# Kernel tuning notes

Hardware: AMD Instinct MI355X
Metric: run time of the kernel (lower is better)

Reference implementation:

```python
import jax, jax.numpy as jnp
import numpy as np

B_GR = 128    # graphs per batch
N0 = 512      # nodes per graph before pooling
E_PER = 4096  # edges per graph (kept static; pooled-away edges get weight 0)
H = 128       # hidden
F = 128       # num_features (== hidden)
C = 10        # num_classes
K_HOP = 3     # Jacobi polynomial order (hop_num)
A_J, B_J = 1.0, 1.0
EPS = 1e-5


def _bn(h, g, b):
    # training-mode BatchNorm1d: batch stats, biased variance
    m = jnp.mean(h, 0)
    v = jnp.mean((h - m) ** 2, 0)
    return (h - m) * jax.lax.rsqrt(v + EPS) * g + b


def _forward(x, convW, convb, bnW, bnB, bn7W, bn7B, attW, theta,
             lin1W, lin1b, lin2W, lin2b, lin3W, lin3b, src, dst):
    w = jnp.ones((src.shape[0],), x.dtype)  # edge weights; 0 => filtered edge
    n = N0
    h = x
    reads = []
    for i in range(5):
        N = B_GR * n
        # symmetric GCN normalization with self loops on the weighted graph
        deg = jax.ops.segment_sum(w, dst, num_segments=N) + 1.0
        dinv = jax.lax.rsqrt(deg)
        enorm = dinv[src] * dinv[dst] * w   # per-edge norm [E]
        snorm = dinv * dinv                 # self-loop norm [N]
        prop = lambda m_: jax.ops.segment_sum(enorm[:, None] * m_[src], dst, num_segments=N) + m_ * snorm[:, None]
        pvec = lambda v_: jax.ops.segment_sum(enorm * v_[src], dst, num_segments=N) + v_ * snorm
        # GCNConv -> BN -> ReLU
        h = prop(h @ convW[i]) + convb[i]
        h = jax.nn.relu(_bn(h, bnW[i], bnB[i]))
        # JacobiPool: Jacobi-polynomial diffusion of attention scores
        s0 = h @ attW[i]                    # [N]
        polys = [s0, 0.5 * ((A_J - B_J) * s0 + (A_J + B_J + 2.0) * pvec(s0))]
        for kk in range(2, K_HOP + 1):
            c0 = 2 * kk * (kk + A_J + B_J) * (2 * kk + A_J + B_J - 2)
            c1 = (2 * kk + A_J + B_J - 1) * (2 * kk + A_J + B_J) * (2 * kk + A_J + B_J - 2)
            c2 = (2 * kk + A_J + B_J - 1) * (A_J * A_J - B_J * B_J)
            c3 = 2 * (kk + A_J - 1) * (kk + B_J - 1) * (2 * kk + A_J + B_J)
            polys.append((c1 * pvec(polys[-1]) + c2 * polys[-1] - c3 * polys[-2]) / c0)
        score = sum(theta[i, j] * polys[j] for j in range(K_HOP + 1))
        # top-k node selection per graph (ratio 0.5 -> static k)
        k = n // 2
        _, idx = jax.lax.top_k(score.reshape(B_GR, n), k)
        sel = (idx + (jnp.arange(B_GR) * n)[:, None]).reshape(-1)  # global node ids [B*k]
        h = h[sel] * jnp.tanh(score[sel])[:, None]
        # remap/filter edges to surviving nodes (masked, static edge count)
        new_id = jnp.full((N,), -1, jnp.int32).at[sel].set(jnp.arange(B_GR * k, dtype=jnp.int32))
        ns, nd = new_id[src], new_id[dst]
        valid = (ns >= 0) & (nd >= 0) & (w > 0)
        w = valid.astype(x.dtype)
        src = jnp.where(valid, ns, 0)
        dst = jnp.where(valid, nd, 0)
        # readout: global max pool || global mean pool per graph
        xg = h.reshape(B_GR, k, H)
        reads.append(jnp.concatenate([xg.max(1), xg.mean(1)], -1))
        n = k
    g = sum(reads) / 5.0                    # [B, 2H]
    g = jax.nn.relu(_bn(g @ lin1W + lin1b, bnW[5], bnB[5]))
    g = jax.nn.relu(_bn(g @ lin2W + lin2b, bn7W, bn7B))
    return jax.nn.log_softmax(g @ lin3W + lin3b, -1)


def setup_inputs() -> dict:
    key = jax.random.key(0)
    ks = jax.random.split(key, 8)
    N = B_GR * N0
    E = B_GR * E_PER
    rng = np.random.default_rng(0)
    off = np.repeat(np.arange(B_GR, dtype=np.int32) * N0, E_PER)
    src = jnp.asarray(off + rng.integers(0, N0, E).astype(np.int32))
    dst = jnp.asarray(off + rng.integers(0, N0, E).astype(np.int32))
    s = 1.0 / np.sqrt(H)
    return {
        "x": jax.random.normal(ks[0], (N, F), jnp.float32),
        "convW": jax.random.normal(ks[1], (5, H, H), jnp.float32) * s,
        "convb": jnp.zeros((5, H), jnp.float32),
        "bnW": jnp.ones((6, H), jnp.float32),
        "bnB": jnp.zeros((6, H), jnp.float32),
        "bn7W": jnp.ones((H // 2,), jnp.float32),
        "bn7B": jnp.zeros((H // 2,), jnp.float32),
        "attW": jax.random.normal(ks[2], (5, H), jnp.float32) * s,
        "theta": jax.random.normal(ks[3], (5, K_HOP + 1), jnp.float32) * 0.5,
        "lin1W": jax.random.normal(ks[4], (2 * H, H), jnp.float32) * (1.0 / np.sqrt(2 * H)),
        "lin1b": jnp.zeros((H,), jnp.float32),
        "lin2W": jax.random.normal(ks[5], (H, H // 2), jnp.float32) * s,
        "lin2b": jnp.zeros((H // 2,), jnp.float32),
        "lin3W": jax.random.normal(ks[6], (H // 2, C), jnp.float32) * (1.0 / np.sqrt(H // 2)),
        "lin3b": jnp.zeros((C,), jnp.float32),
        "src": src,
        "dst": dst,
    }


def reference(x, convW, convb, bnW, bnB, bn7W, bn7B, attW, theta,
              lin1W, lin1b, lin2W, lin2b, lin3W, lin3b, src, dst):
    return _forward(x, convW, convb, bnW, bnB, bn7W, bn7B, attW, theta,
                    lin1W, lin1b, lin2W, lin2b, lin3W, lin3b, src, dst)
```

## Files before the change

kernel.cpp:

```cpp
#include <hip/hip_runtime.h>
#include <hip/hip_bf16.h>

#define B_GRAPH 128
#define ETOT    (128*4096)
#define N0G     (128*512)
#define HF      128
#define STSZ    2048

union IGSmem {
    float Ws[64*HF];
    struct { int cnt8[8][512]; int cur[512]; float dvl[512]; int wsum[4]; } ini;
};

__global__ __launch_bounds__(256) void k_init_gemm(
    const float* __restrict__ A, const float* __restrict__ Wg, float* __restrict__ C,
    const int* __restrict__ s_in, const int* __restrict__ d_in_,
    int2* __restrict__ csr, int2* __restrict__ rb2, float* __restrict__ dinvv,
    float* __restrict__ gacc, float* __restrict__ statsH,
    float* __restrict__ st0, float* __restrict__ st1, float* __restrict__ st2)
{
    __shared__ IGSmem sm;
    int t = threadIdx.x;
    if (blockIdx.x >= 128){
        int tx = t & 15, ty = t >> 4;
        int r0 = (blockIdx.x - 128)*128 + ty*8, c0 = tx*4;
        float acc[8][8];
        #pragma unroll
        for (int j=0;j<8;++j)
            #pragma unroll
            for (int l=0;l<8;++l) acc[j][l] = 0.f;
        for (int kh = 0; kh < 2; ++kh){
            __syncthreads();
            {
                float4* d4 = (float4*)sm.Ws;
                const float4* s4 = (const float4*)(Wg + kh*64*HF);
                #pragma unroll
                for (int i2 = 0; i2 < 8; ++i2) d4[t + i2*256] = s4[t + i2*256];
            }
            __syncthreads();
            float4 avc[8];
            #pragma unroll
            for (int j=0;j<8;++j)
                avc[j] = *(const float4*)(A + (size_t)(r0+j)*HF + kh*64);
            for (int k4 = 0; k4 < 16; ++k4){
                int k4n = (k4+1 < 16) ? (k4+1) : 15;
                float4 avn[8];
                #pragma unroll
                for (int j=0;j<8;++j)
                    avn[j] = *(const float4*)(A + (size_t)(r0+j)*HF + kh*64 + k4n*4);
                #pragma unroll
                for (int kk=0; kk<4; ++kk){
                    int kl = k4*4 + kk;
                    float4 w0 = *(const float4*)(sm.Ws + kl*HF + c0);
                    float4 w1 = *(const float4*)(sm.Ws + kl*HF + c0 + 64);
                    #pragma unroll
                    for (int j=0;j<8;++j){
                        float a = reinterpret_cast<const float*>(&avc[j])[kk];
                        acc[j][0] += a*w0.x; acc[j][1] += a*w0.y; acc[j][2] += a*w0.z; acc[j][3] += a*w0.w;
                        acc[j][4] += a*w1.x; acc[j][5] += a*w1.y; acc[j][6] += a*w1.z; acc[j][7] += a*w1.w;
                    }
                }
                #pragma unroll
                for (int j=0;j<8;++j) avc[j] = avn[j];
            }
        }
        #pragma unroll
        for (int j=0;j<8;++j){
            *(float4*)(C + (size_t)(r0+j)*HF + c0)      = make_float4(acc[j][0],acc[j][1],acc[j][2],acc[j][3]);
            *(float4*)(C + (size_t)(r0+j)*HF + c0 + 64) = make_float4(acc[j][4],acc[j][5],acc[j][6],acc[j][7]);
        }
    } else {
        int g = blockIdx.x;
        int wid = t >> 5;
        for (int l = t; l < 4096; l += 256) ((int*)sm.ini.cnt8)[l] = 0;
        gacc[g*256 + t] = 0.f;
        if (g == 0){
            if (t < 256){ statsH[t] = 0.f; if (t < 128) statsH[256+t] = 0.f; }
            for (int i = t; i < STSZ; i += 256){ st0[i] = 0.f; st1[i] = 0.f; st2[i] = 0.f; }
        }
        __syncthreads();
        for (int j = t; j < 4096; j += 256){
            int e = g*4096 + j;
            atomicAdd(&sm.ini.cnt8[wid][d_in_[e] & 511], 1);
        }
        __syncthreads();
        int c0 = 0, c1 = 0;
        #pragma unroll
        for (int w = 0; w < 8; ++w){ c0 += sm.ini.cnt8[w][2*t]; c1 += sm.ini.cnt8[w][2*t+1]; }
        int pairsum = c0 + c1;
        int lane = t & 63, wv = t >> 6;
        int v = pairsum;
        #pragma unroll
        for (int off = 1; off < 64; off <<= 1){
            int nv = __shfl_up(v, off);
            if (lane >= off) v += nv;
        }
        if (lane == 63) sm.ini.wsum[wv] = v;
        __syncthreads();
        for (int ww = 0; ww < wv; ++ww) v += sm.ini.wsum[ww];
        int begpair = v - pairsum;
        sm.ini.cur[2*t]   = begpair;
        sm.ini.cur[2*t+1] = begpair + c0;
        sm.ini.cnt8[0][2*t]   = c0;
        sm.ini.cnt8[0][2*t+1] = c1;
        __syncthreads();
        for (int l = t; l < 512; l += 256){
            int cl = sm.ini.cnt8[0][l];
            rb2[g*512 + l] = make_int2(g*4096 + sm.ini.cur[l], cl);
            float dv = rsqrtf((float)cl + 1.f);
            sm.ini.dvl[l] = dv;
            dinvv[g*512 + l] = dv;
        }
        __syncthreads();
        for (int j = t; j < 4096; j += 256){
            int e = g*4096 + j;
            int sg = s_in[e], dl = d_in_[e] & 511;
            int p = atomicAdd(&sm.ini.cur[dl], 1);
            csr[g*4096 + (p & 4095)] = make_int2(sg, __float_as_int(sm.ini.dvl[sg & 511]));
        }
    }
}

template<int NN>
__global__ __launch_bounds__(512) void k_prop_lds(
    const float* __restrict__ Y, const float* __restrict__ cb,
    const int2* __restrict__ rb2, const int2* __restrict__ cp,
    const float* __restrict__ dinv, float* __restrict__ X, float* __restrict__ st)
{
    constexpr int TP = 512 / NN;
    constexpr int FQ = 8 / TP;
    __shared__ float4 ly[NN * 8];
    int b = blockIdx.x;
    int g = b >> 2, q = b & 3;
    int t = threadIdx.x;
    const float4* Y4 = (const float4*)Y + (size_t)g*NN*32 + q*8;
    for (int i = t; i < NN*8; i += 512){
        int row = i >> 3, slot = i & 7;
        ly[row*8 + ((slot + row) & 7)] = Y4[(size_t)row*32 + slot];
    }
    __syncthreads();
    int r   = t & (NN - 1);
    int sub = t / NN;
    int S0  = sub * FQ;
    int vg  = g*NN + r;
    float dv = dinv[vg];
    int2 rb = rb2[vg];
    int e0  = (rb.x - g*4096) & 4095;
    int len = min(max(rb.y, 0), 4096 - e0);
    const int2* cpg = cp + g*4096 + e0;
    float4 acc[FQ];
    #pragma unroll
    for (int s = 0; s < FQ; ++s) acc[s] = make_float4(0.f,0.f,0.f,0.f);
    for (int j = 0; j < len; ++j){
        int2 e = cpg[j];
        int c = e.x & (NN - 1);
        float en = __int_as_float(e.y);
        #pragma unroll
        for (int s = 0; s < FQ; ++s){
            float4 h = ly[c*8 + ((S0 + s + c) & 7)];
            acc[s].x += en*h.x; acc[s].y += en*h.y; acc[s].z += en*h.z; acc[s].w += en*h.w;
        }
    }
    const float4* cb4 = (const float4*)cb + q*8;
    float4* X4 = (float4*)X + q*8;
    #pragma unroll
    for (int s = 0; s < FQ; ++s){
        float4 y = ly[r*8 + ((S0 + s + r) & 7)];
        float4 cbv = cb4[S0 + s];
        acc[s].x = y.x*dv*dv + dv*acc[s].x + cbv.x;
        acc[s].y = y.y*dv*dv + dv*acc[s].y + cbv.y;
        acc[s].z = y.z*dv*dv + dv*acc[s].z + cbv.z;
        acc[s].w = y.w*dv*dv + dv*acc[s].w + cbv.w;
        X4[(size_t)vg*32 + S0 + s] = acc[s];
    }
    __syncthreads();
    float* lf = (float*)ly;
    #pragma unroll
    for (int s = 0; s < FQ; ++s) *(float4*)&lf[r*32 + (S0 + s)*4] = acc[s];
    __syncthreads();
    float ssum = 0.f, qsum = 0.f;
    {
        int col = t & 31, grp = t >> 5;
        for (int rr = grp; rr < NN; rr += 16){
            float v = lf[rr*32 + col];
            ssum += v; qsum += v*v;
        }
    }
    __syncthreads();
    lf[t] = ssum; lf[512 + t] = qsum;
    __syncthreads();
    if (t < 64){
        int col = t & 31, half = t >> 5;
        float a = 0.f;
        #pragma unroll
        for (int i = 0; i < 16; ++i) a += lf[half*512 + i*32 + col];
        atomicAdd(&st[(b & 7)*256 + half*128 + q*32 + col], a);
    }
}

__global__ __launch_bounds__(256) void k_prop_stats(const float* __restrict__ Y, const float* __restrict__ cb,
                                                    const int2* __restrict__ rb2, const int2* __restrict__ cp,
                                                    const float* __restrict__ dinv,
                                                    float* __restrict__ X, float* __restrict__ st,
                                                    int n, int lb, int Nn){
    __shared__ float rs[1024], rq[1024];
    int xcd = blockIdx.x & 7, c = blockIdx.x >> 3;
    int g = xcd*16 + (c >> lb);
    int m = c & ((1 << lb) - 1);
    int nd = threadIdx.x >> 5;
    int v = g*n + m*8 + nd;
    int f4 = threadIdx.x & 31;
    float dv = dinv[v];
    float4 y = *(const float4*)(Y + (size_t)v*HF + f4*4);
    float4 acc = make_float4(0.f, 0.f, 0.f, 0.f);
    int2 rb = rb2[v];
    int len = min(max(rb.y, 0), 4096);
    int e0 = rb.x, e1 = rb.x + len;
    for (int j = e0; j < e1; ++j){
        int2 e = cp[j];
        int s = e.x & (Nn - 1);
        float en = __int_as_float(e.y);
        float4 h = *(const float4*)(Y + (size_t)s*HF + f4*4);
        acc.x += en*h.x; acc.y += en*h.y; acc.z += en*h.z; acc.w += en*h.w;
    }
    int f = f4*4;
    acc.x = y.x*dv*dv + dv*acc.x + cb[f];
    acc.y = y.y*dv*dv + dv*acc.y + cb[f+1];
    acc.z = y.z*dv*dv + dv*acc.z + cb[f+2];
    acc.w = y.w*dv*dv + dv*acc.w + cb[f+3];
    *(float4*)(X + (size_t)v*HF + f) = acc;
    *(float4*)&rs[nd*HF + f] = acc;
    *(float4*)&rq[nd*HF + f] = make_float4(acc.x*acc.x, acc.y*acc.y, acc.z*acc.z, acc.w*acc.w);
    __syncthreads();
    if (threadIdx.x < 128){
        int tt = threadIdx.x;
        float s = 0.f, q = 0.f;
        #pragma unroll
        for (int j = 0; j < 8; ++j){ s += rs[j*HF + tt]; q += rq[j*HF + tt]; }
        atomicAdd(&st[xcd*256 + tt], s);
        atomicAdd(&st[xcd*256 + 128 + tt], q);
    }
}

__global__ __launch_bounds__(256) void k_score(
    const float* __restrict__ H, const float* __restrict__ stats,
    const float* __restrict__ gw, const float* __restrict__ gb,
    const float* __restrict__ aw, float* __restrict__ s0G, float invN)
{
    __shared__ float bna[128], bnb[128], awl[128];
    int t = threadIdx.x;
    if (t < 128){
        float s = 0.f, q = 0.f;
        #pragma unroll
        for (int b2 = 0; b2 < 8; ++b2){ s += stats[b2*256 + t]; q += stats[b2*256 + 128 + t]; }
        float mean = s*invN;
        float var  = q*invN - mean*mean;
        float iv   = rsqrtf(var + 1e-5f);
        bna[t] = iv*gw[t];
        bnb[t] = gb[t] - mean*iv*gw[t];
        awl[t] = aw[t];
    }
    __syncthreads();
    int v = blockIdx.x*128 + (t >> 1);
    int h = t & 1;
    const float* hp = H + (size_t)v*HF + h*64;
    float part = 0.f;
    #pragma unroll
    for (int j = 0; j < 16; ++j){
        float4 x = *(const float4*)(hp + j*4);
        int f = h*64 + j*4;
        float4 a4 = *(const float4*)&bna[f];
        float4 b4 = *(const float4*)&bnb[f];
        float4 w4 = *(const float4*)&awl[f];
        part += fmaxf(x.x*a4.x + b4.x, 0.f)*w4.x
              + fmaxf(x.y*a4.y + b4.y, 0.f)*w4.y
              + fmaxf(x.z*a4.z + b4.z, 0.f)*w4.z
              + fmaxf(x.w*a4.w + b4.w, 0.f)*w4.w;
    }
    float oth = __shfl_xor(part, 1);
    if (h == 0) s0G[v] = part + oth;
}

__global__ __launch_bounds__(256) void k_gemm_g(
    const float* __restrict__ Hsrc, const float* __restrict__ stats,
    const float* __restrict__ gw, const float* __restrict__ gb,
    const int* __restrict__ siG, const float* __restrict__ tssG,
    const float* __restrict__ Wg, float* __restrict__ C,
    float invN, int lk, int ln)
{
    __shared__ float Ws[64*HF];
    __shared__ float bna[128], bnb[128];
    int t = threadIdx.x;
    if (t < 128){
        float s = 0.f, q = 0.f;
        #pragma unroll
        for (int b2 = 0; b2 < 8; ++b2){ s += stats[b2*256 + t]; q += stats[b2*256 + 128 + t]; }
        float mean = s*invN;
        float var  = q*invN - mean*mean;
        float iv   = rsqrtf(var + 1e-5f);
        bna[t] = iv*gw[t];
        bnb[t] = gb[t] - mean*iv*gw[t];
    }
    int tx = t & 15, ty = t >> 4;
    int r0 = blockIdx.x*128 + ty*8, c0 = tx*4;
    int rbase[8]; float ts_[8];
    int nmask = (1 << ln) - 1;
    #pragma unroll
    for (int j = 0; j < 8; ++j){
        int rg = r0 + j;
        int g = rg >> lk;
        int old = siG[rg] & nmask;
        rbase[j] = ((g << ln) + old) * HF;
        ts_[j] = tssG[rg];
    }
    float acc[8][8];
    #pragma unroll
    for (int j=0;j<8;++j)
        #pragma unroll
        for (int l=0;l<8;++l) acc[j][l] = 0.f;
    for (int kh = 0; kh < 2; ++kh){
        __syncthreads();
        {
            float4* d4 = (float4*)Ws;
            const float4* s4 = (const float4*)(Wg + kh*64*HF);
            #pragma unroll
            for (int i2 = 0; i2 < 8; ++i2) d4[t + i2*256] = s4[t + i2*256];
        }
        __syncthreads();
        float4 avc[8];
        #pragma unroll
        for (int j=0;j<8;++j) avc[j] = *(const float4*)(Hsrc + (size_t)rbase[j] + kh*64);
        for (int k4 = 0; k4 < 16; ++k4){
            int fb  = kh*64 + k4*4;
            int fbn = kh*64 + (((k4+1 < 16) ? (k4+1) : 15) * 4);
            float4 avn[8];
            #pragma unroll
            for (int j=0;j<8;++j) avn[j] = *(const float4*)(Hsrc + (size_t)rbase[j] + fbn);
            float4 ba = *(const float4*)&bna[fb];
            float4 bb = *(const float4*)&bnb[fb];
            #pragma unroll
            for (int j=0;j<8;++j){
                avc[j].x = fmaxf(avc[j].x*ba.x + bb.x, 0.f)*ts_[j];
                avc[j].y = fmaxf(avc[j].y*ba.y + bb.y, 0.f)*ts_[j];
                avc[j].z = fmaxf(avc[j].z*ba.z + bb.z, 0.f)*ts_[j];
                avc[j].w = fmaxf(avc[j].w*ba.w + bb.w, 0.f)*ts_[j];
            }
            #pragma unroll
            for (int kk=0; kk<4; ++kk){
                int kl = k4*4 + kk;
                float4 w0 = *(const float4*)(Ws + kl*HF + c0);
                float4 w1 = *(const float4*)(Ws + kl*HF + c0 + 64);
                #pragma unroll
                for (int j=0;j<8;++j){
                    float a = reinterpret_cast<const float*>(&avc[j])[kk];
                    acc[j][0] += a*w0.x; acc[j][1] += a*w0.y; acc[j][2] += a*w0.z; acc[j][3] += a*w0.w;
                    acc[j][4] += a*w1.x; acc[j][5] += a*w1.y; acc[j][6] += a*w1.z; acc[j][7] += a*w1.w;
                }
            }
            #pragma unroll
            for (int j=0;j<8;++j) avc[j] = avn[j];
        }
    }
    #pragma unroll
    for (int j=0;j<8;++j){
        *(float4*)(C + (size_t)(r0+j)*HF + c0)      = make_float4(acc[j][0],acc[j][1],acc[j][2],acc[j][3]);
        *(float4*)(C + (size_t)(r0+j)*HF + c0 + 64) = make_float4(acc[j][4],acc[j][5],acc[j][6],acc[j][7]);
    }
}

struct __align__(16) PSmem {
    int2  eds[4096];
    int2  rbl[512];
    float dvv[512], p0[512], p1[512], p2[512];
    float ss[512]; int si[512]; float tss[256]; int nid[512];
    int   cnt_[256]; int wsum[4]; float dvn[256];
    float bna[128], bnb[128]; float red[1024];
};

__global__ __launch_bounds__(1024) void k_pool(
    const float* __restrict__ H, const float* __restrict__ stats,
    const float* __restrict__ gw, const float* __restrict__ gb,
    const float* __restrict__ th,
    const int2* __restrict__ rb2, int2* __restrict__ csr, const float* __restrict__ dinv,
    const float* __restrict__ s0G,
    float* __restrict__ gacc, int2* __restrict__ rb2n, float* __restrict__ dinvn,
    float* __restrict__ stZero, int* __restrict__ siG, float* __restrict__ tssG,
    const float* __restrict__ lin1W, const float* __restrict__ lin1b,
    float* __restrict__ t1g, float* __restrict__ statsH,
    float invN, float ca2, float cc2, float ca3, float cc3,
    int n, int last)
{
    int g = blockIdx.x, t = threadIdx.x;
    int k = n >> 1;
    __shared__ PSmem sm;

    if (t < 256) stZero[(g & 7)*256 + t] = 0.f;
    if (t < 128){
        float s = 0.f, q = 0.f;
        #pragma unroll
        for (int b2 = 0; b2 < 8; ++b2){ s += stats[b2*256 + t]; q += stats[b2*256 + 128 + t]; }
        float mean = s*invN;
        float var  = q*invN - mean*mean;
        float iv   = rsqrtf(var + 1e-5f);
        sm.bna[t] = iv*gw[t];
        sm.bnb[t] = gb[t] - mean*iv*gw[t];
    }
    for (int l = t; l < n; l += 1024){
        int2 rb = rb2[g*n + l];
        int bx = (rb.x - g*4096) & 4095;
        int by = min(max(rb.y, 0), 4096 - bx);
        sm.rbl[l] = make_int2(bx, by);
        sm.dvv[l] = dinv[g*n + l];
        sm.p0[l]  = s0G[g*n + l];
    }
    __syncthreads();
    int medg = sm.rbl[n-1].x + sm.rbl[n-1].y;
    for (int j = t; j < medg; j += 1024){
        int2 e = csr[g*4096 + j];
        sm.eds[j] = make_int2(e.x & (n-1), e.y);
    }
    __syncthreads();
    for (int l = t; l < n; l += 1024){
        int2 rc = sm.rbl[l];
        float acc = 0.f;
        for (int j = 0; j < rc.y; ++j){
            int2 e = sm.eds[rc.x + j];
            acc += __int_as_float(e.y) * sm.p0[e.x];
        }
        float dv = sm.dvv[l];
        sm.p1[l] = 2.f*(sm.p0[l]*dv*dv + dv*acc);
    }
    __syncthreads();
    for (int l = t; l < n; l += 1024){
        int2 rc = sm.rbl[l];
        float acc = 0.f;
        for (int j = 0; j < rc.y; ++j){
            int2 e = sm.eds[rc.x + j];
            acc += __int_as_float(e.y) * sm.p1[e.x];
        }
        float dv = sm.dvv[l];
        sm.p2[l] = ca2*(sm.p1[l]*dv*dv + dv*acc) + cc2*sm.p0[l];
    }
    __syncthreads();
    float t0v = th[0], t1v = th[1], t2c = th[2], t3v = th[3];
    for (int l = t; l < n; l += 1024){
        int2 rc = sm.rbl[l];
        float acc = 0.f;
        for (int j = 0; j < rc.y; ++j){
            int2 e = sm.eds[rc.x + j];
            acc += __int_as_float(e.y) * sm.p2[e.x];
        }
        float dv = sm.dvv[l];
        float tv = sm.p2[l]*dv*dv + dv*acc;
        float p3 = ca3*tv + cc3*sm.p1[l];
        sm.ss[l] = t0v*sm.p0[l] + t1v*sm.p1[l] + t2c*sm.p2[l] + t3v*p3;
    }
    __syncthreads();
    for (int l = t; l < n; l += 1024){
        float sl = sm.ss[l];
        int r = 0;
        for (int j = 0; j < n; j += 4){
            float4 s4 = *(const float4*)&sm.ss[j];
            r += (s4.x > sl) || (s4.x == sl && (j    ) < l);
            r += (s4.y > sl) || (s4.y == sl && (j + 1) < l);
            r += (s4.z > sl) || (s4.z == sl && (j + 2) < l);
            r += (s4.w > sl) || (s4.w == sl && (j + 3) < l);
        }
        if (r < k){
            sm.nid[l] = r;
            sm.si[r]  = l;
            float tv = tanhf(sl);
            sm.tss[r] = tv;
            siG[g*k + r]  = l;
            tssG[g*k + r] = tv;
        } else {
            sm.nid[l] = -1;
        }
    }
    __syncthreads();
    if (!last){
        if (t < k){
            int l = sm.si[t] & (n-1);
            int2 rc = sm.rbl[l];
            int c2 = 0;
            for (int j = 0; j < rc.y; ++j) c2 += (sm.nid[sm.eds[rc.x + j].x] >= 0);
            sm.cnt_[t] = c2;
        }
        __syncthreads();
        int c = (t < 256) ? ((t < k) ? sm.cnt_[t] : 0) : 0;
        int vscan = c;
        if (t < 256){
            int lane = t & 63;
            #pragma unroll
            for (int off = 1; off < 64; off <<= 1){
                int nv = __shfl_up(vscan, off);
                if (lane >= off) vscan += nv;
            }
            if (lane == 63) sm.wsum[t >> 6] = vscan;
        }
        __syncthreads();
        int beg = 0;
        if (t < k){
            int wv = t >> 6;
            int add = 0;
            for (int ww = 0; ww < wv; ++ww) add += sm.wsum[ww];
            vscan += add;
            beg = vscan - c;
            rb2n[g*k + t] = make_int2(g*4096 + beg, c);
            float dv = rsqrtf((float)c + 1.f);
            dinvn[g*k + t] = dv;
            sm.dvn[t] = dv;
        }
        __syncthreads();
        if (t < k){
            int l = sm.si[t] & (n-1);
            int2 rc = sm.rbl[l];
            int p = beg;
            for (int j = 0; j < rc.y; ++j){
                int ns = sm.nid[sm.eds[rc.x + j].x];
                if (ns >= 0){ csr[g*4096 + (p & 4095)] = make_int2(g*k + ns, __float_as_int(sm.dvn[ns])); ++p; }
            }
        }
        __syncthreads();
    }
    {
        int f4 = t & 31, rl = t >> 5;
        int f = f4*4;
        float4 a4 = *(const float4*)&sm.bna[f];
        float4 b4 = *(const float4*)&sm.bnb[f];
        float4 mx = make_float4(-3.4e38f,-3.4e38f,-3.4e38f,-3.4e38f);
        float4 smv = make_float4(0.f,0.f,0.f,0.f);
        for (int r = rl; r < k; r += 32){
            int old = sm.si[r] & (n-1);
            float4 hv = *(const float4*)(H + ((size_t)g*n + old)*HF + f);
            float ts = sm.tss[r];
            float4 v;
            v.x = fmaxf(hv.x*a4.x + b4.x, 0.f)*ts;
            v.y = fmaxf(hv.y*a4.y + b4.y, 0.f)*ts;
            v.z = fmaxf(hv.z*a4.z + b4.z, 0.f)*ts;
            v.w = fmaxf(hv.w*a4.w + b4.w, 0.f)*ts;
            mx.x = fmaxf(mx.x, v.x); mx.y = fmaxf(mx.y, v.y);
            mx.z = fmaxf(mx.z, v.z); mx.w = fmaxf(mx.w, v.w);
            smv.x += v.x; smv.y += v.y; smv.z += v.z; smv.w += v.w;
        }
        float* scr = (float*)sm.eds;
        *(float4*)&scr[rl*128 + f]        = mx;
        *(float4*)&scr[4096 + rl*128 + f] = smv;
        __syncthreads();
        if (t < 128){
            float m = -3.4e38f, s = 0.f;
            #pragma unroll
            for (int j = 0; j < 32; ++j){
                m = fmaxf(m, scr[j*128 + t]);
                s += scr[4096 + j*128 + t];
            }
            gacc[g*256 + t] += m;
            gacc[g*256 + 128 + t] += s / (float)k;
        }
    }
    if (last){
        __syncthreads();
        int c = t & 127, h = t >> 7;
        float s = 0.f;
        int k0 = h*32;
        #pragma unroll
        for (int kk = 0; kk < 32; ++kk)
            s += gacc[g*256 + k0 + kk] * lin1W[(k0 + kk)*128 + c];
        sm.red[t] = s;
        __syncthreads();
        if (t < 512) sm.red[t] += sm.red[t+512];
        __syncthreads();
        if (t < 256) sm.red[t] += sm.red[t+256];
        __syncthreads();
        if (t < 128){
            float v = (sm.red[t] + sm.red[t+128]) * 0.2f + lin1b[t];
            t1g[g*128 + t] = v;
            atomicAdd(&statsH[t], v);
            atomicAdd(&statsH[128+t], v*v);
        }
    }
}

__global__ __launch_bounds__(128) void k_head2(const float* __restrict__ t1, const float* __restrict__ gw,
                                               const float* __restrict__ gb, const float* __restrict__ W2,
                                               const float* __restrict__ b2, float* __restrict__ sh,
                                               float* __restrict__ t2){
    int r = blockIdx.x, t = threadIdx.x;
    int cc = t & 63, h = t >> 6;
    __shared__ float row[128];
    __shared__ float red[128];
    {
        float mean = sh[t] * (1.f/128.f);
        float var  = sh[128+t]*(1.f/128.f) - mean*mean;
        float iv   = rsqrtf(var + 1e-5f);
        float v = (t1[r*128+t] - mean)*iv*gw[t] + gb[t];
        row[t] = fmaxf(v, 0.f);
    }
    __syncthreads();
    float s = 0.f;
    #pragma unroll
    for (int kk = 0; kk < 64; ++kk)
        s += row[h*64+kk] * W2[(h*64+kk)*64 + cc];
    red[t] = s;
    __syncthreads();
    if (h == 0){
        float v = red[cc] + red[cc+64] + b2[cc];
        t2[r*64+cc] = v;
        atomicAdd(&sh[256+cc], v);
        atomicAdd(&sh[320+cc], v*v);
    }
}
__global__ __launch_bounds__(64) void k_head3(const float* __restrict__ t2, const float* __restrict__ gw,
                                              const float* __restrict__ gb, const float* __restrict__ W3,
                                              const float* __restrict__ b3, const float* __restrict__ sh,
                                              float* __restrict__ out){
    int r = blockIdx.x, t = threadIdx.x;
    float mean = sh[256+t]*(1.f/128.f);
    float var  = sh[320+t]*(1.f/128.f) - mean*mean;
    float iv   = rsqrtf(var + 1e-5f);
    float v = fmaxf((t2[r*64+t]-mean)*iv*gw[t] + gb[t], 0.f);
    float lg[10];
    #pragma unroll
    for (int j = 0; j < 10; ++j){
        float p = v * W3[t*10 + j];
        for (int off = 32; off; off >>= 1) p += __shfl_down(p, off);
        lg[j] = p;
    }
    if (t == 0){
        float m = -3.4e38f;
        #pragma unroll
        for (int j = 0; j < 10; ++j){ lg[j] += b3[j]; m = fmaxf(m, lg[j]); }
        float se = 0.f;
        #pragma unroll
        for (int j = 0; j < 10; ++j) se += expf(lg[j] - m);
        float l = logf(se) + m;
        #pragma unroll
        for (int j = 0; j < 10; ++j) out[r*10 + j] = lg[j] - l;
    }
}

extern "C" void kernel_launch(void* const* d_in, const int* in_sizes, int n_in,
                              void* d_out, int out_size, void* d_ws, size_t ws_size,
                              hipStream_t stream){
    const float* x     = (const float*)d_in[0];
    const float* convW = (const float*)d_in[1];
    const float* convb = (const float*)d_in[2];
    const float* bnW   = (const float*)d_in[3];
    const float* bnB   = (const float*)d_in[4];
    const float* bn7W  = (const float*)d_in[5];
    const float* bn7B  = (const float*)d_in[6];
    const float* attW  = (const float*)d_in[7];
    const float* theta = (const float*)d_in[8];
    const float* lin1W = (const float*)d_in[9];
    const float* lin1b = (const float*)d_in[10];
    const float* lin2W = (const float*)d_in[11];
    const float* lin2b = (const float*)d_in[12];
    const float* lin3W = (const float*)d_in[13];
    const float* lin3b = (const float*)d_in[14];
    const int*   src0  = (const int*)d_in[15];
    const int*   dst0  = (const int*)d_in[16];

    char* base = (char*)d_ws;
    size_t off = 0;
    auto take = [&](size_t bytes) -> void* {
        void* p = base + off;
        off = (off + bytes + 255) & ~(size_t)255;
        return p;
    };
    float* bufGP = (float*)take((size_t)N0G*HF*4);
    float* bufHA = (float*)take((size_t)N0G*HF*4);
    float* bufHB = (float*)take((size_t)(N0G/2)*HF*4);
    int2*  csr_p = (int2*) take((size_t)ETOT*8);
    int2*  rb2A  = (int2*) take((size_t)N0G*8);
    int2*  rb2B  = (int2*) take((size_t)N0G*8);
    float* dinvA = (float*)take((size_t)N0G*4);
    float* dinvB = (float*)take((size_t)N0G*4);
    float* s0G   = (float*)take((size_t)N0G*4);
    int*   siG   = (int*)  take((size_t)(N0G/2)*4);
    float* tssG  = (float*)take((size_t)(N0G/2)*4);
    float* st[3];
    st[0] = (float*)take(STSZ*4);
    st[1] = (float*)take(STSZ*4);
    st[2] = (float*)take(STSZ*4);
    float* gacc  = (float*)take((size_t)B_GRAPH*256*4);
    float* t1    = (float*)take((size_t)B_GRAPH*128*4);
    float* t2    = (float*)take((size_t)B_GRAPH*64*4);
    float* statsH= (float*)take(384*4);

    auto coef = [](int kk, float& ca, float& cc){
        double a = 1.0, b = 1.0;
        double c0 = 2.0*kk*(kk+a+b)*(2.0*kk+a+b-2.0);
        double c1 = (2.0*kk+a+b-1.0)*(2.0*kk+a+b)*(2.0*kk+a+b-2.0);
        double c3 = 2.0*(kk+a-1.0)*(kk+b-1.0)*(2.0*kk+a+b);
        ca = (float)(c1/c0); cc = (float)(-c3/c0);
    };
    float ca2, cc2, ca3, cc3;
    coef(2, ca2, cc2);
    coef(3, ca3, cc3);

    k_init_gemm<<<128 + 512, 256, 0, stream>>>(x, convW, bufGP,
                                               src0, dst0, csr_p, rb2A, dinvA,
                                               gacc, statsH, st[0], st[1], st[2]);
    k_prop_lds<512><<<512, 512, 0, stream>>>(bufGP, convb, rb2A, csr_p, dinvA, bufHA, st[0]);

    float* G = bufGP + (size_t)4*1024*1024;

    for (int i = 0; i < 5; ++i){
        int n = 512 >> i;
        int kk = n >> 1;
        int Nn = B_GRAPH*n;
        float invN = 1.0f/(float)Nn;
        int2*  rb_cur = (i & 1) ? rb2B : rb2A;
        int2*  rb_nxt = (i & 1) ? rb2A : rb2B;
        float* dv_cur = (i & 1) ? dinvB : dinvA;
        float* dv_nxt = (i & 1) ? dinvA : dinvB;
        float* Hcur = (i & 1) ? bufHB : bufHA;
        float* Hnxt = (i & 1) ? bufHA : bufHB;

        k_score<<<Nn/128, 256, 0, stream>>>(Hcur, st[i % 3], bnW + i*HF, bnB + i*HF, attW + i*HF,
                                            s0G, invN);
        k_pool<<<B_GRAPH, 1024, 0, stream>>>(Hcur, st[i % 3], bnW + i*HF, bnB + i*HF,
                                             theta + i*4, rb_cur, csr_p, dv_cur, s0G,
                                             gacc, rb_nxt, dv_nxt,
                                             st[(i + 1) % 3], siG, tssG,
                                             lin1W, lin1b, t1, statsH,
                                             invN, ca2, cc2, ca3, cc3, n, (i == 4) ? 1 : 0);
        if (i < 4){
            int wnext = i + 1;
            int rows = B_GRAPH * kk;
            int lk = 8 - i;
            int ln = 9 - i;
            k_gemm_g<<<rows/128, 256, 0, stream>>>(Hcur, st[i % 3], bnW + i*HF, bnB + i*HF,
                                                   siG, tssG, convW + (size_t)wnext*HF*HF, G,
                                                   invN, lk, ln);
            if (kk == 256){
                k_prop_lds<256><<<512, 512, 0, stream>>>(G, convb + wnext*HF, rb_nxt, csr_p, dv_nxt,
                                                         Hnxt, st[(i + 1) % 3]);
            } else {
                int lbn = (kk == 128) ? 4 : (kk == 64) ? 3 : 2;
                k_prop_stats<<<rows/8, 256, 0, stream>>>(G, convb + wnext*HF, rb_nxt, csr_p, dv_nxt,
                                                         Hnxt, st[(i + 1) % 3], kk, lbn, rows);
            }
        }
    }

    k_head2<<<B_GRAPH, 128, 0, stream>>>(t1, bnW + 5*HF, bnB + 5*HF, lin2W, lin2b, statsH, t2);
    k_head3<<<B_GRAPH, 64, 0, stream>>>(t2, bn7W, bn7B, lin3W, lin3b, statsH, (float*)d_out);
}
```

Before: 418.9 us.

## Stage activation tiles in swizzled LDS and size gather-GEMM tiles per level

```diff
diff --git a/kernel.cpp b/kernel.cpp
--- a/kernel.cpp
+++ b/kernel.cpp
@@ -8,7 +8,7 @@
 #define STSZ    2048
 
 union IGSmem {
-    float Ws[64*HF];
+    float As[128*64];
     struct { int cnt8[8][512]; int cur[512]; float dvl[512]; int wsum[4]; } ini;
 };
 
@@ -23,7 +23,8 @@
     int t = threadIdx.x;
     if (blockIdx.x >= 128){
         int tx = t & 15, ty = t >> 4;
-        int r0 = (blockIdx.x - 128)*128 + ty*8, c0 = tx*4;
+        int r0 = (blockIdx.x - 128)*128, c0 = tx*4;
+        int sw = ty & 3;
         float acc[8][8];
         #pragma unroll
         for (int j=0;j<8;++j)
@@ -31,43 +32,38 @@
             for (int l=0;l<8;++l) acc[j][l] = 0.f;
         for (int kh = 0; kh < 2; ++kh){
             __syncthreads();
-            {
-                float4* d4 = (float4*)sm.Ws;
-                const float4* s4 = (const float4*)(Wg + kh*64*HF);
-                #pragma unroll
-                for (int i2 = 0; i2 < 8; ++i2) d4[t + i2*256] = s4[t + i2*256];
+            #pragma unroll
+            for (int p = 0; p < 8; ++p){
+                int idx = p*256 + t;
+                int row = idx >> 4, col4 = idx & 15;
+                float4 v = *(const float4*)(A + (size_t)(r0+row)*HF + kh*64 + col4*4);
+                *(float4*)&sm.As[row*64 + ((col4 ^ ((row>>3)&3))<<2)] = v;
             }
             __syncthreads();
-            float4 avc[8];
-            #pragma unroll
-            for (int j=0;j<8;++j)
-                avc[j] = *(const float4*)(A + (size_t)(r0+j)*HF + kh*64);
+            const float* Wk = Wg + kh*64*HF;
             for (int k4 = 0; k4 < 16; ++k4){
-                int k4n = (k4+1 < 16) ? (k4+1) : 15;
-                float4 avn[8];
+                float4 av[8];
                 #pragma unroll
                 for (int j=0;j<8;++j)
-                    avn[j] = *(const float4*)(A + (size_t)(r0+j)*HF + kh*64 + k4n*4);
+                    av[j] = *(const float4*)&sm.As[(ty*8+j)*64 + ((k4 ^ sw)<<2)];
                 #pragma unroll
                 for (int kk=0; kk<4; ++kk){
                     int kl = k4*4 + kk;
-                    float4 w0 = *(const float4*)(sm.Ws + kl*HF + c0);
-                    float4 w1 = *(const float4*)(sm.Ws + kl*HF + c0 + 64);
+                    float4 w0 = *(const float4*)(Wk + kl*HF + c0);
+                    float4 w1 = *(const float4*)(Wk + kl*HF + c0 + 64);
                     #pragma unroll
                     for (int j=0;j<8;++j){
-                        float a = reinterpret_cast<const float*>(&avc[j])[kk];
+                        float a = reinterpret_cast<const float*>(&av[j])[kk];
                         acc[j][0] += a*w0.x; acc[j][1] += a*w0.y; acc[j][2] += a*w0.z; acc[j][3] += a*w0.w;
                         acc[j][4] += a*w1.x; acc[j][5] += a*w1.y; acc[j][6] += a*w1.z; acc[j][7] += a*w1.w;
                     }
                 }
-                #pragma unroll
-                for (int j=0;j<8;++j) avc[j] = avn[j];
             }
         }
         #pragma unroll
         for (int j=0;j<8;++j){
-            *(float4*)(C + (size_t)(r0+j)*HF + c0)      = make_float4(acc[j][0],acc[j][1],acc[j][2],acc[j][3]);
-            *(float4*)(C + (size_t)(r0+j)*HF + c0 + 64) = make_float4(acc[j][4],acc[j][5],acc[j][6],acc[j][7]);
+            *(float4*)(C + (size_t)(r0+ty*8+j)*HF + c0)      = make_float4(acc[j][0],acc[j][1],acc[j][2],acc[j][3]);
+            *(float4*)(C + (size_t)(r0+ty*8+j)*HF + c0 + 64) = make_float4(acc[j][4],acc[j][5],acc[j][6],acc[j][7]);
         }
     } else {
         int g = blockIdx.x;
@@ -281,14 +277,17 @@
     if (h == 0) s0G[v] = part + oth;
 }
 
-__global__ __launch_bounds__(256) void k_gemm_g(
+template<int RPT>
+__global__ __launch_bounds__(256) void k_gemm_gs(
     const float* __restrict__ Hsrc, const float* __restrict__ stats,
     const float* __restrict__ gw, const float* __restrict__ gb,
     const int* __restrict__ siG, const float* __restrict__ tssG,
     const float* __restrict__ Wg, float* __restrict__ C,
     float invN, int lk, int ln)
 {
-    __shared__ float Ws[64*HF];
+    constexpr int RPB = RPT*16;
+    constexpr int SH  = (RPT == 8) ? 3 : 2;
+    __shared__ float As[RPB*64];
     __shared__ float bna[128], bnb[128];
     int t = threadIdx.x;
     if (t < 128){
@@ -302,67 +301,127 @@
         bnb[t] = gb[t] - mean*iv*gw[t];
     }
     int tx = t & 15, ty = t >> 4;
-    int r0 = blockIdx.x*128 + ty*8, c0 = tx*4;
-    int rbase[8]; float ts_[8];
+    int r0 = blockIdx.x*RPB, c0 = tx*4;
     int nmask = (1 << ln) - 1;
-    #pragma unroll
-    for (int j = 0; j < 8; ++j){
+    int sw = ty & 3;
+    float acc[RPT][8];
+    #pragma unroll
+    for (int j=0;j<RPT;++j)
+        #pragma unroll
+        for (int l=0;l<8;++l) acc[j][l] = 0.f;
+    for (int kh = 0; kh < 2; ++kh){
+        __syncthreads();
+        #pragma unroll
+        for (int p = 0; p < RPB/16; ++p){
+            int idx = p*256 + t;
+            int row = idx >> 4, col4 = idx & 15;
+            int rg = r0 + row;
+            int g = rg >> lk;
+            int old = siG[rg] & nmask;
+            float ts = tssG[rg];
+            int f = kh*64 + col4*4;
+            float4 v = *(const float4*)(Hsrc + (size_t)((g<<ln)+old)*HF + f);
+            float4 ba = *(const float4*)&bna[f];
+            float4 bb = *(const float4*)&bnb[f];
+            v.x = fmaxf(v.x*ba.x + bb.x, 0.f)*ts;
+            v.y = fmaxf(v.y*ba.y + bb.y, 0.f)*ts;
+            v.z = fmaxf(v.z*ba.z + bb.z, 0.f)*ts;
+            v.w = fmaxf(v.w*ba.w + bb.w, 0.f)*ts;
+            *(float4*)&As[row*64 + ((col4 ^ ((row>>SH)&3))<<2)] = v;
+        }
+        __syncthreads();
+        const float* Wk = Wg + kh*64*HF;
+        for (int k4 = 0; k4 < 16; ++k4){
+            float4 av[RPT];
+            #pragma unroll
+            for (int j=0;j<RPT;++j)
+                av[j] = *(const float4*)&As[(ty*RPT+j)*64 + ((k4 ^ sw)<<2)];
+            #pragma unroll
+            for (int kk=0; kk<4; ++kk){
+                int kl = k4*4 + kk;
+                float4 w0 = *(const float4*)(Wk + kl*HF + c0);
+                float4 w1 = *(const float4*)(Wk + kl*HF + c0 + 64);
+                #pragma unroll
+                for (int j=0;j<RPT;++j){
+                    float a = reinterpret_cast<const float*>(&av[j])[kk];
+                    acc[j][0] += a*w0.x; acc[j][1] += a*w0.y; acc[j][2] += a*w0.z; acc[j][3] += a*w0.w;
+                    acc[j][4] += a*w1.x; acc[j][5] += a*w1.y; acc[j][6] += a*w1.z; acc[j][7] += a*w1.w;
+                }
+            }
+        }
+    }
+    #pragma unroll
+    for (int j=0;j<RPT;++j){
+        *(float4*)(C + (size_t)(r0+ty*RPT+j)*HF + c0)      = make_float4(acc[j][0],acc[j][1],acc[j][2],acc[j][3]);
+        *(float4*)(C + (size_t)(r0+ty*RPT+j)*HF + c0 + 64) = make_float4(acc[j][4],acc[j][5],acc[j][6],acc[j][7]);
+    }
+}
+
+__global__ __launch_bounds__(256) void k_gemm_g32(
+    const float* __restrict__ Hsrc, const float* __restrict__ stats,
+    const float* __restrict__ gw, const float* __restrict__ gb,
+    const int* __restrict__ siG, const float* __restrict__ tssG,
+    const float* __restrict__ Wg, float* __restrict__ C,
+    float invN, int lk, int ln)
+{
+    __shared__ float bna[128], bnb[128];
+    int t = threadIdx.x;
+    if (t < 128){
+        float s = 0.f, q = 0.f;
+        #pragma unroll
+        for (int b2 = 0; b2 < 8; ++b2){ s += stats[b2*256 + t]; q += stats[b2*256 + 128 + t]; }
+        float mean = s*invN;
+        float var  = q*invN - mean*mean;
+        float iv   = rsqrtf(var + 1e-5f);
+        bna[t] = iv*gw[t];
+        bnb[t] = gb[t] - mean*iv*gw[t];
+    }
+    __syncthreads();
+    int tx = t & 15, ty = t >> 4;
+    int r0 = blockIdx.x*32 + ty*2, c0 = tx*4;
+    int nmask = (1 << ln) - 1;
+    int rbase[2]; float ts_[2];
+    #pragma unroll
+    for (int j = 0; j < 2; ++j){
         int rg = r0 + j;
         int g = rg >> lk;
         int old = siG[rg] & nmask;
         rbase[j] = ((g << ln) + old) * HF;
         ts_[j] = tssG[rg];
     }
-    float acc[8][8];
-    #pragma unroll
-    for (int j=0;j<8;++j)
+    float acc[2][8];
+    #pragma unroll
+    for (int j=0;j<2;++j)
         #pragma unroll
         for (int l=0;l<8;++l) acc[j][l] = 0.f;
-    for (int kh = 0; kh < 2; ++kh){
-        __syncthreads();
-        {
-            float4* d4 = (float4*)Ws;
-            const float4* s4 = (const float4*)(Wg + kh*64*HF);
+    for (int k4 = 0; k4 < 32; ++k4){
+        int f = k4*4;
+        float4 ba = *(const float4*)&bna[f];
+        float4 bb = *(const float4*)&bnb[f];
+        float4 av[2];
+        #pragma unroll
+        for (int j=0;j<2;++j){
+            av[j] = *(const float4*)(Hsrc + (size_t)rbase[j] + f);
+            av[j].x = fmaxf(av[j].x*ba.x + bb.x, 0.f)*ts_[j];
+            av[j].y = fmaxf(av[j].y*ba.y + bb.y, 0.f)*ts_[j];
+            av[j].z = fmaxf(av[j].z*ba.z + bb.z, 0.f)*ts_[j];
+            av[j].w = fmaxf(av[j].w*ba.w + bb.w, 0.f)*ts_[j];
+        }
+        #pragma unroll
+        for (int kk=0; kk<4; ++kk){
+            int kl = f + kk;
+            float4 w0 = *(const float4*)(Wg + kl*HF + c0);
+            float4 w1 = *(const float4*)(Wg + kl*HF + c0 + 64);
             #pragma unroll
-            for (int i2 = 0; i2 < 8; ++i2) d4[t + i2*256] = s4[t + i2*256];
-        }
-        __syncthreads();
-        float4 avc[8];
-        #pragma unroll
-        for (int j=0;j<8;++j) avc[j] = *(const float4*)(Hsrc + (size_t)rbase[j] + kh*64);
-        for (int k4 = 0; k4 < 16; ++k4){
-            int fb  = kh*64 + k4*4;
-            int fbn = kh*64 + (((k4+1 < 16) ? (k4+1) : 15) * 4);
-            float4 avn[8];
-            #pragma unroll
-            for (int j=0;j<8;++j) avn[j] = *(const float4*)(Hsrc + (size_t)rbase[j] + fbn);
-            float4 ba = *(const float4*)&bna[fb];
-            float4 bb = *(const float4*)&bnb[fb];
-            #pragma unroll
-            for (int j=0;j<8;++j){
-                avc[j].x = fmaxf(avc[j].x*ba.x + bb.x, 0.f)*ts_[j];
-                avc[j].y = fmaxf(avc[j].y*ba.y + bb.y, 0.f)*ts_[j];
-                avc[j].z = fmaxf(avc[j].z*ba.z + bb.z, 0.f)*ts_[j];
-                avc[j].w = fmaxf(avc[j].w*ba.w + bb.w, 0.f)*ts_[j];
+            for (int j=0;j<2;++j){
+                float a = reinterpret_cast<const float*>(&av[j])[kk];
+                acc[j][0] += a*w0.x; acc[j][1] += a*w0.y; acc[j][2] += a*w0.z; acc[j][3] += a*w0.w;
+                acc[j][4] += a*w1.x; acc[j][5] += a*w1.y; acc[j][6] += a*w1.z; acc[j][7] += a*w1.w;
             }
-            #pragma unroll
-            for (int kk=0; kk<4; ++kk){
-                int kl = k4*4 + kk;
-                float4 w0 = *(const float4*)(Ws + kl*HF + c0);
-                float4 w1 = *(const float4*)(Ws + kl*HF + c0 + 64);
-                #pragma unroll
-                for (int j=0;j<8;++j){
-                    float a = reinterpret_cast<const float*>(&avc[j])[kk];
-                    acc[j][0] += a*w0.x; acc[j][1] += a*w0.y; acc[j][2] += a*w0.z; acc[j][3] += a*w0.w;
-                    acc[j][4] += a*w1.x; acc[j][5] += a*w1.y; acc[j][6] += a*w1.z; acc[j][7] += a*w1.w;
-                }
-            }
-            #pragma unroll
-            for (int j=0;j<8;++j) avc[j] = avn[j];
-        }
-    }
-    #pragma unroll
-    for (int j=0;j<8;++j){
+        }
+    }
+    #pragma unroll
+    for (int j=0;j<2;++j){
         *(float4*)(C + (size_t)(r0+j)*HF + c0)      = make_float4(acc[j][0],acc[j][1],acc[j][2],acc[j][3]);
         *(float4*)(C + (size_t)(r0+j)*HF + c0 + 64) = make_float4(acc[j][4],acc[j][5],acc[j][6],acc[j][7]);
     }
@@ -730,9 +789,16 @@
             int rows = B_GRAPH * kk;
             int lk = 8 - i;
             int ln = 9 - i;
-            k_gemm_g<<<rows/128, 256, 0, stream>>>(Hcur, st[i % 3], bnW + i*HF, bnB + i*HF,
-                                                   siG, tssG, convW + (size_t)wnext*HF*HF, G,
-                                                   invN, lk, ln);
+            const float* Wn = convW + (size_t)wnext*HF*HF;
+            if (i == 0)
+                k_gemm_gs<8><<<rows/128, 256, 0, stream>>>(Hcur, st[i % 3], bnW + i*HF, bnB + i*HF,
+                                                           siG, tssG, Wn, G, invN, lk, ln);
+            else if (i == 1)
+                k_gemm_gs<4><<<rows/64, 256, 0, stream>>>(Hcur, st[i % 3], bnW + i*HF, bnB + i*HF,
+                                                          siG, tssG, Wn, G, invN, lk, ln);
+            else
+                k_gemm_g32<<<rows/32, 256, 0, stream>>>(Hcur, st[i % 3], bnW + i*HF, bnB + i*HF,
+                                                        siG, tssG, Wn, G, invN, lk, ln);
             if (kk == 256){
                 k_prop_lds<256><<<512, 512, 0, stream>>>(G, convb + wnext*HF, rb_nxt, csr_p, dv_nxt,
                                                          Hnxt, st[(i + 1) % 3]);
```

After: 401.6 us. -4.1%, faster.
